# Kernel optimization log

Hardware: AMD Instinct MI355X
Metric: run time of the kernel (lower is better)

The kernel has to match this reference:

```python
import jax, jax.numpy as jnp
import numpy as np

DIM = 1280
HEADS = 16
HD = DIM // HEADS  # 80
NSEG = 8
LSEG = 1024
SEQ = NSEG * LSEG  # 8192


def _rotate_half(x):
    x1, x2 = jnp.split(x, 2, axis=-1)
    return jnp.concatenate([-x2, x1], axis=-1)


def setup_inputs() -> dict:
    key = jax.random.key(0)
    ks = jax.random.split(key, 6)
    hidden_states = jax.random.normal(ks[0], (SEQ, DIM), dtype=jnp.float32)
    # rotary embedding table: per-position angles over head_dim
    inv_freq = 1.0 / (10000.0 ** (np.arange(0, HD, 2, dtype=np.float32) / HD))
    pos = np.arange(SEQ, dtype=np.float32)
    freqs = np.outer(pos, inv_freq)                    # [SEQ, HD/2]
    emb = np.concatenate([freqs, freqs], axis=-1)      # [SEQ, HD]
    cos = jnp.asarray(np.cos(emb), dtype=jnp.float32)
    sin = jnp.asarray(np.sin(emb), dtype=jnp.float32)
    w_scale = 1.0 / np.sqrt(DIM)
    qkv_w = jax.random.normal(ks[1], (DIM, 3 * DIM), dtype=jnp.float32) * w_scale
    qkv_b = jax.random.normal(ks[2], (3 * DIM,), dtype=jnp.float32) * 0.02
    proj_w = jax.random.normal(ks[3], (DIM, DIM), dtype=jnp.float32) * w_scale
    proj_b = jax.random.normal(ks[4], (DIM,), dtype=jnp.float32) * 0.02
    cu_seqlens = jnp.arange(NSEG + 1, dtype=jnp.int32) * LSEG
    return {
        "hidden_states": hidden_states,
        "cos": cos,
        "sin": sin,
        "qkv_w": qkv_w,
        "qkv_b": qkv_b,
        "proj_w": proj_w,
        "proj_b": proj_b,
        "cu_seqlens": cu_seqlens,
    }


def reference(hidden_states, cos, sin, qkv_w, qkv_b, proj_w, proj_b, cu_seqlens):
    S, D = hidden_states.shape
    n_seg = cu_seqlens.shape[0] - 1          # static
    L = S // n_seg                            # equal-length packed segments
    # fused QKV projection: [S, 3D] -> q, k, v each [S, H, hd]
    qkv = hidden_states @ qkv_w + qkv_b
    q, k, v = (t.reshape(S, HEADS, HD) for t in jnp.split(qkv, 3, axis=-1))
    # RoPE (computed in fp32, as in apply_rotary_pos_emb_vision)
    c = cos.astype(jnp.float32)[:, None, :]   # [S, 1, hd]
    s = sin.astype(jnp.float32)[:, None, :]
    qf = q.astype(jnp.float32)
    kf = k.astype(jnp.float32)
    q = (qf * c + _rotate_half(qf) * s).astype(q.dtype)
    k = (kf * c + _rotate_half(kf) * s).astype(k.dtype)
    # block-diagonal varlen attention == independent attention per segment
    qs = q.reshape(n_seg, L, HEADS, HD)
    ks = k.reshape(n_seg, L, HEADS, HD)
    vs = v.reshape(n_seg, L, HEADS, HD)
    scale = HD ** -0.5
    scores = jnp.einsum("nqhd,nkhd->nhqk", qs, ks) * scale
    probs = jax.nn.softmax(scores.astype(jnp.float32), axis=-1).astype(qs.dtype)
    out = jnp.einsum("nhqk,nkhd->nqhd", probs, vs)     # [n, L, H, hd]
    out = out.reshape(S, D)
    return out @ proj_w + proj_b
```

## Files before the change

kernel.cpp:

```cpp
#include <hip/hip_runtime.h>

#define SEQ   8192
#define DIM   1280
#define HEADS 16
#define HD    80
#define LSEG  1024
#define QKVD  3840

typedef unsigned short USHORT;
typedef __attribute__((ext_vector_type(8))) short bf16x8;
typedef __attribute__((ext_vector_type(4))) float f32x4;
typedef __attribute__((ext_vector_type(4))) USHORT u16x4;
typedef __attribute__((ext_vector_type(2))) unsigned uint2v;

#define CSF  0.16129832f
#define DTHR 71.554175f

__device__ __forceinline__ USHORT f2bf(float x) {
  unsigned u = __float_as_uint(x);
  u += 0x7fffu + ((u >> 16) & 1u);
  return (USHORT)(u >> 16);
}
__device__ __forceinline__ float bf2f(USHORT b) {
  return __uint_as_float(((unsigned)b) << 16);
}
__device__ __forceinline__ void gload16(const void* g, void* l) {
  __builtin_amdgcn_global_load_lds(
      (const __attribute__((address_space(1))) void*)g,
      (__attribute__((address_space(3))) void*)l, 16, 0, 0);
}
__device__ __forceinline__ unsigned cvtpk(float a, float b) {
  unsigned d;
  asm("v_cvt_pk_bf16_f32 %0, %1, %2" : "=v"(d) : "v"(a), "v"(b));
  return d;
}

__global__ __launch_bounds__(256) void conv_f2b(const float* __restrict__ in,
                                                USHORT* __restrict__ out, int n4) {
  int i = blockIdx.x * 256 + threadIdx.x;
  if (i >= n4) return;
  float4 v = reinterpret_cast<const float4*>(in)[i];
  USHORT* o = out + (size_t)i * 4;
  o[0] = f2bf(v.x); o[1] = f2bf(v.y); o[2] = f2bf(v.z); o[3] = f2bf(v.w);
}

__global__ __launch_bounds__(256) void conv_transpose(const float* __restrict__ W,
                                                      USHORT* __restrict__ Th,
                                                      int K, int N) {
  __shared__ float t[32][33];
  const int n0 = blockIdx.x * 32, k0 = blockIdx.y * 32;
  const int c = threadIdx.x & 31, r0 = threadIdx.x >> 5;
  for (int r = r0; r < 32; r += 8) t[r][c] = W[(size_t)(k0 + r) * N + n0 + c];
  __syncthreads();
  for (int r = r0; r < 32; r += 8)
    Th[(size_t)(n0 + r) * K + k0 + c] = f2bf(t[c][r]);
}

__global__ __launch_bounds__(256) void vtrans(const USHORT* __restrict__ qkv,
                                              USHORT* __restrict__ VtG) {
  __shared__ USHORT t[32][33];
  const int c0 = blockIdx.x * 32, s0 = blockIdx.y * 32;
  const int c = threadIdx.x & 31, r0 = threadIdx.x >> 5;
  for (int r = r0; r < 32; r += 8)
    t[r][c] = qkv[(size_t)(s0 + r) * QKVD + 2 * DIM + c0 + c];
  __syncthreads();
  for (int r = r0; r < 32; r += 8)
    VtG[(size_t)(c0 + r) * SEQ + s0 + c] = t[c][r];
}

template <int OUTBF>
__global__ __launch_bounds__(256) void mfma_gemm(
    const USHORT* __restrict__ Ah, const USHORT* __restrict__ Bh,
    const float* __restrict__ bias, void* __restrict__ Cout,
    int M, int N, int K, int lda) {
  __shared__ __align__(16) USHORT AhL[2][8192];
  __shared__ __align__(16) USHORT BhL[2][8192];

  const int tid = threadIdx.x;
  const int l = tid & 63;
  const int w = tid >> 6;
  const int nrow = M >> 7;
  const int nwg = nrow * (N >> 7);
  const int orig = blockIdx.x;
  const int wg = (orig & 7) * (nwg >> 3) + (orig >> 3);
  const int row0 = (wg % nrow) << 7;
  const int col0 = (wg / nrow) << 7;
  const int wr = (w >> 1) << 6;
  const int wc = (w & 1) << 6;

  const f32x4 fz = {0.f, 0.f, 0.f, 0.f};
  f32x4 acc[4][4];
#pragma unroll
  for (int m = 0; m < 4; ++m)
#pragma unroll
    for (int n = 0; n < 4; ++n) acc[m][n] = fz;

  const int fr = l & 15;
  const int g = l >> 4;

  const int NT = K >> 6;

  auto stage = [&](int t, int b) {
    const int k0 = t << 6;
#pragma unroll
    for (int i = 0; i < 4; ++i) {
      const int u = (w * 4 + i) * 64 + l;
      const int row = u >> 3;
      const int c = (u & 7) ^ (row & 7);
      gload16(Ah + (size_t)(row0 + row) * lda + k0 + c * 8,
              &AhL[b][(w * 4 + i) * 512]);
      gload16(Bh + (size_t)(col0 + row) * K + k0 + c * 8,
              &BhL[b][(w * 4 + i) * 512]);
    }
  };

  stage(0, 0);
  stage(1, 1);

  for (int t = 0; t < NT; ++t) {
    const int cur = t & 1;
    asm volatile("s_waitcnt vmcnt(8)" ::: "memory");
    __builtin_amdgcn_sched_barrier(0);
    __builtin_amdgcn_s_barrier();
    __builtin_amdgcn_sched_barrier(0);
    bf16x8 ah[2][4], bh[2][4];
#pragma unroll
    for (int ks = 0; ks < 2; ++ks)
#pragma unroll
      for (int m = 0; m < 4; ++m) {
        const int sl = (((ks << 2) + g) ^ (fr & 7)) << 3;
        ah[ks][m] = *(const bf16x8*)&AhL[cur][(wr + m * 16 + fr) * 64 + sl];
        bh[ks][m] = *(const bf16x8*)&BhL[cur][(wc + m * 16 + fr) * 64 + sl];
      }
    asm volatile("s_waitcnt lgkmcnt(0)" ::: "memory");
    __builtin_amdgcn_sched_barrier(0);
    __builtin_amdgcn_s_barrier();
    __builtin_amdgcn_sched_barrier(0);
    const int tn = (t + 2 < NT) ? t + 2 : t;
    stage(tn, cur);
    __builtin_amdgcn_sched_barrier(0);
    __builtin_amdgcn_s_setprio(1);
#pragma unroll
    for (int ks = 0; ks < 2; ++ks)
#pragma unroll
      for (int m = 0; m < 4; ++m)
#pragma unroll
        for (int n = 0; n < 4; ++n)
          acc[m][n] = __builtin_amdgcn_mfma_f32_16x16x32_bf16(
              ah[ks][m], bh[ks][n], acc[m][n], 0, 0, 0);
    __builtin_amdgcn_s_setprio(0);
  }

  asm volatile("s_waitcnt vmcnt(0)" ::: "memory");

  float bv[4];
#pragma unroll
  for (int n = 0; n < 4; ++n) bv[n] = bias[col0 + wc + n * 16 + fr];
#pragma unroll
  for (int m = 0; m < 4; ++m)
#pragma unroll
    for (int n = 0; n < 4; ++n)
#pragma unroll
      for (int r = 0; r < 4; ++r) {
        const float v = acc[m][n][r] + bv[n];
        const int row = row0 + wr + m * 16 + (l >> 4) * 4 + r;
        const int col = col0 + wc + n * 16 + fr;
        if (OUTBF)
          ((USHORT*)Cout)[(size_t)row * N + col] = f2bf(v);
        else
          ((float*)Cout)[(size_t)row * N + col] = v;
      }
}

__global__ __launch_bounds__(256) void rope_b(USHORT* __restrict__ qkv,
                                              const float* __restrict__ cosb,
                                              const float* __restrict__ sinb) {
  int idx = blockIdx.x * 256 + threadIdx.x;
  const int d4 = (idx % 10) * 4;
  int t = idx / 10;
  const int h = t % HEADS;
  t /= HEADS;
  const int qk = t & 1;
  const int s = t >> 1;
  USHORT* base = qkv + (size_t)s * QKVD + qk * DIM + h * HD;
  const u16x4 x1 = *(const u16x4*)&base[d4];
  const u16x4 x2 = *(const u16x4*)&base[d4 + 40];
  const f32x4 c1 = *(const f32x4*)&cosb[s * HD + d4];
  const f32x4 s1 = *(const f32x4*)&sinb[s * HD + d4];
  const f32x4 c2 = *(const f32x4*)&cosb[s * HD + d4 + 40];
  const f32x4 s2 = *(const f32x4*)&sinb[s * HD + d4 + 40];
  u16x4 o1, o2;
#pragma unroll
  for (int j = 0; j < 4; ++j) {
    const float a = bf2f(x1[j]), b = bf2f(x2[j]);
    o1[j] = f2bf(a * c1[j] - b * s1[j]);
    o2[j] = f2bf(b * c2[j] + a * s2[j]);
  }
  *(u16x4*)&base[d4] = o1;
  *(u16x4*)&base[d4 + 40] = o2;
}

__global__ void zero_ws(uint4* z) {
  z[threadIdx.x] = uint4{0u, 0u, 0u, 0u};
}

__global__ __launch_bounds__(256) void attn_mfma6(const USHORT* __restrict__ qkv,
                                                  const USHORT* __restrict__ VtG,
                                                  const USHORT* __restrict__ zbuf,
                                                  USHORT* __restrict__ aoB) {
  const int h = blockIdx.y;
  const int bx = blockIdx.x;
  const int qb = (bx & 7) * 8 + (bx >> 3);
  const int s0 = qb * 128;
  const int k0g = (s0 / LSEG) * LSEG;
  const int tid = threadIdx.x;
  const int w = tid >> 6, l = tid & 63;
  const int g = l >> 4, fr = l & 15;
  const int q0 = s0 + w * 32;

  __shared__ __align__(16) USHORT Kl[2][64 * 128];
  __shared__ __align__(16) USHORT Vl[2][6144];
  __shared__ __align__(16) USHORT Pl[4][32 * 72];

  bf16x8 qb_frag[2][3];
#pragma unroll
  for (int nt2 = 0; nt2 < 2; ++nt2)
#pragma unroll
    for (int ks = 0; ks < 3; ++ks)
      qb_frag[nt2][ks] = *(const bf16x8*)
          &qkv[(size_t)(q0 + nt2 * 16 + fr) * QKVD + h * HD + ks * 32 + g * 8];

  const f32x4 fz = {0.f, 0.f, 0.f, 0.f};
  f32x4 oacc[2][5];
#pragma unroll
  for (int m = 0; m < 2; ++m)
#pragma unroll
    for (int n = 0; n < 5; ++n) oacc[m][n] = fz;
  float m_run[2] = {-3e38f, -3e38f};
  float l_run[2] = {0.f, 0.f};

  auto stageKV = [&](int kb, int b) {
    const size_t krow0 = (size_t)(k0g + kb * 64);
#pragma unroll
    for (int i = 0; i < 4; ++i) {
      const int t = (w * 4 + i) * 64 + l;
      const int row = t >> 4, c2 = t & 15, c = c2 ^ (row & 7);
      const USHORT* src =
          (c < 10) ? &qkv[(krow0 + row) * QKVD + DIM + h * HD + c * 8] : zbuf;
      gload16(src, &Kl[b][(w * 4 + i) * 512]);
    }
#pragma unroll
    for (int i = 0; i < 3; ++i) {
      const int u = (w * 3 + i) * 64 + l;
      const int s = u / 9, r8 = u - s * 9;
      const USHORT* src = (r8 < 8 && s < 80)
          ? &VtG[(size_t)(h * HD + s) * SEQ + krow0 + r8 * 8] : zbuf;
      gload16(src, &Vl[b][(w * 3 + i) * 512]);
    }
  };

  stageKV(0, 0);
  stageKV(1, 1);

  for (int kb = 0; kb < 16; ++kb) {
    const int cur = kb & 1;
    asm volatile("s_waitcnt vmcnt(7)" ::: "memory");
    __builtin_amdgcn_sched_barrier(0);
    __builtin_amdgcn_s_barrier();
    __builtin_amdgcn_sched_barrier(0);

    f32x4 sc[4][2];
#pragma unroll
    for (int m = 0; m < 4; ++m)
#pragma unroll
      for (int nt2 = 0; nt2 < 2; ++nt2) sc[m][nt2] = fz;
#pragma unroll
    for (int ks = 0; ks < 3; ++ks)
#pragma unroll
      for (int m = 0; m < 4; ++m) {
        const bf16x8 kbf = *(const bf16x8*)
            &Kl[cur][(m * 16 + fr) * 128 + ((4 * ks + g) ^ (fr & 7)) * 8];
#pragma unroll
        for (int nt2 = 0; nt2 < 2; ++nt2)
          sc[m][nt2] = __builtin_amdgcn_mfma_f32_16x16x32_bf16(
              kbf, qb_frag[nt2][ks], sc[m][nt2], 0, 0, 0);
      }

    float rmax[2];
#pragma unroll
    for (int nt2 = 0; nt2 < 2; ++nt2) {
      float mx = -3e38f;
#pragma unroll
      for (int m = 0; m < 4; ++m)
#pragma unroll
        for (int j = 0; j < 4; ++j) mx = fmaxf(mx, sc[m][nt2][j]);
      mx = fmaxf(mx, __shfl_xor(mx, 16));
      mx = fmaxf(mx, __shfl_xor(mx, 32));
      rmax[nt2] = mx;
    }
    const bool need =
        (rmax[0] > m_run[0] + DTHR) || (rmax[1] > m_run[1] + DTHR);
    if (__any(need)) {
      float fac[2];
#pragma unroll
      for (int nt2 = 0; nt2 < 2; ++nt2) {
        const float mn = fmaxf(m_run[nt2], rmax[nt2]);
        fac[nt2] = exp2f((m_run[nt2] - mn) * CSF);
        m_run[nt2] = mn;
        l_run[nt2] *= fac[nt2];
      }
#pragma unroll
      for (int mt2 = 0; mt2 < 2; ++mt2)
#pragma unroll
        for (int j = 0; j < 4; ++j) {
          const float fb = __shfl(fac[mt2], 20 * g + j);
#pragma unroll
          for (int nt = 0; nt < 5; ++nt) oacc[mt2][nt][j] *= fb;
        }
    }
#pragma unroll
    for (int nt2 = 0; nt2 < 2; ++nt2) {
      const float mcs = m_run[nt2] * CSF;
      float ps = 0.f;
#pragma unroll
      for (int m = 0; m < 4; ++m) {
        float p[4];
#pragma unroll
        for (int j = 0; j < 4; ++j) {
          p[j] = exp2f(sc[m][nt2][j] * CSF - mcs);
          ps += p[j];
        }
        const uint2v pw = {cvtpk(p[0], p[1]), cvtpk(p[2], p[3])};
        *(uint2v*)&Pl[w][(nt2 * 16 + fr) * 72 + m * 16 + g * 4] = pw;
      }
      ps += __shfl_xor(ps, 16);
      ps += __shfl_xor(ps, 32);
      l_run[nt2] += ps;
    }

#pragma unroll
    for (int ks = 0; ks < 2; ++ks) {
      bf16x8 pa[2];
#pragma unroll
      for (int mt2 = 0; mt2 < 2; ++mt2)
        pa[mt2] = *(const bf16x8*)&Pl[w][(mt2 * 16 + fr) * 72 + ks * 32 + g * 8];
#pragma unroll
      for (int nt = 0; nt < 5; ++nt) {
        const bf16x8 vb =
            *(const bf16x8*)&Vl[cur][(nt * 16 + fr) * 72 + ks * 32 + g * 8];
#pragma unroll
        for (int mt2 = 0; mt2 < 2; ++mt2)
          oacc[mt2][nt] = __builtin_amdgcn_mfma_f32_16x16x32_bf16(
              pa[mt2], vb, oacc[mt2][nt], 0, 0, 0);
      }
    }

    __builtin_amdgcn_s_barrier();
    __builtin_amdgcn_sched_barrier(0);
    const int kn = (kb + 2 < 16) ? kb + 2 : kb;
    stageKV(kn, cur);
    __builtin_amdgcn_sched_barrier(0);
  }

  asm volatile("s_waitcnt vmcnt(0)" ::: "memory");

  float linv[2][4];
#pragma unroll
  for (int mt2 = 0; mt2 < 2; ++mt2)
#pragma unroll
    for (int j = 0; j < 4; ++j)
      linv[mt2][j] = 1.f / __shfl(l_run[mt2], 20 * g + j);
#pragma unroll
  for (int mt2 = 0; mt2 < 2; ++mt2)
#pragma unroll
    for (int nt = 0; nt < 5; ++nt)
#pragma unroll
      for (int j = 0; j < 4; ++j) {
        const int row = s0 + w * 32 + mt2 * 16 + g * 4 + j;
        const int col = h * HD + nt * 16 + fr;
        aoB[(size_t)row * QKVD + col] = f2bf(oacc[mt2][nt][j] * linv[mt2][j]);
      }
}

extern "C" void kernel_launch(void* const* d_in, const int* in_sizes, int n_in,
                              void* d_out, int out_size, void* d_ws,
                              size_t ws_size, hipStream_t stream) {
  const float* hs = (const float*)d_in[0];
  const float* cosb = (const float*)d_in[1];
  const float* sinb = (const float*)d_in[2];
  const float* qkv_w = (const float*)d_in[3];
  const float* qkv_b = (const float*)d_in[4];
  const float* proj_w = (const float*)d_in[5];
  const float* proj_b = (const float*)d_in[6];
  char* ws = (char*)d_ws;

  USHORT* qkvB  = (USHORT*)(ws);
  USHORT* hsB   = (USHORT*)(ws + 62914560u);
  USHORT* qkvwT = (USHORT*)(ws + 83886080u);
  USHORT* pwT   = (USHORT*)(ws + 93716480u);
  USHORT* VtG   = hsB;
  USHORT* zbuf  = qkvwT;
  USHORT* aoB   = qkvB + 2 * DIM;

  conv_f2b<<<SEQ * DIM / 4 / 256, 256, 0, stream>>>(hs, hsB, SEQ * DIM / 4);
  conv_transpose<<<dim3(QKVD / 32, DIM / 32), 256, 0, stream>>>(
      qkv_w, qkvwT, DIM, QKVD);
  conv_transpose<<<dim3(DIM / 32, DIM / 32), 256, 0, stream>>>(
      proj_w, pwT, DIM, DIM);

  mfma_gemm<1><<<(SEQ / 128) * (QKVD / 128), 256, 0, stream>>>(
      hsB, qkvwT, qkv_b, qkvB, SEQ, QKVD, DIM, DIM);
  rope_b<<<SEQ * HEADS * 2 * 10 / 256, 256, 0, stream>>>(qkvB, cosb, sinb);
  vtrans<<<dim3(DIM / 32, SEQ / 32), 256, 0, stream>>>(qkvB, VtG);
  zero_ws<<<1, 64, 0, stream>>>((uint4*)zbuf);
  attn_mfma6<<<dim3(SEQ / 128, HEADS), 256, 0, stream>>>(qkvB, VtG, zbuf, aoB);
  mfma_gemm<0><<<(SEQ / 128) * (DIM / 128), 256, 0, stream>>>(
      aoB, pwT, proj_b, d_out, SEQ, DIM, DIM, QKVD);
}
```

Before: 311.6 us.

## Use 256x256-tile 512-thread MFMA GEMM for QKV projection

Adds a new GEMM kernel with 256x256 output tiles, 8 waves per block, 128KB dynamic LDS, double-buffered K=64 staging with XOR swizzle, and uses it for the QKV projection. Larger tiles raise arithmetic intensity and cut global reloads of A and B. The cost is fewer workgroups (480) and higher register and LDS pressure, which may limit occupancy. The launch_bounds(512,2) requests two blocks per CU, which 128KB of LDS per block would not allow.

```diff
diff --git a/kernel.cpp b/kernel.cpp
--- a/kernel.cpp
+++ b/kernel.cpp
@@ -66,6 +66,109 @@
   __syncthreads();
   for (int r = r0; r < 32; r += 8)
     VtG[(size_t)(c0 + r) * SEQ + s0 + c] = t[c][r];
+}
+
+__global__ __launch_bounds__(512, 2) void mfma_gemm256(
+    const USHORT* __restrict__ Ah, const USHORT* __restrict__ Bh,
+    const float* __restrict__ bias, USHORT* __restrict__ Cout,
+    int M, int N, int K, int lda) {
+  extern __shared__ USHORT sm[];
+
+  const int tid = threadIdx.x;
+  const int l = tid & 63;
+  const int w = tid >> 6;
+  const int fr = l & 15;
+  const int g = l >> 4;
+  const int nrow = M >> 8;
+  const int nwg = nrow * (N >> 8);
+  const int orig = blockIdx.x;
+  const int wg = (orig & 7) * (nwg >> 3) + (orig >> 3);
+  const int row0 = (wg % nrow) << 8;
+  const int col0 = (wg / nrow) << 8;
+  const int wr = (w >> 2) << 7;
+  const int wc = (w & 3) << 6;
+
+  const f32x4 fz = {0.f, 0.f, 0.f, 0.f};
+  f32x4 acc[8][4];
+#pragma unroll
+  for (int m = 0; m < 8; ++m)
+#pragma unroll
+    for (int n = 0; n < 4; ++n) acc[m][n] = fz;
+
+  const int NT = K >> 6;
+
+  auto stage = [&](int t, int b) {
+    const int k0 = t << 6;
+#pragma unroll
+    for (int i = 0; i < 4; ++i) {
+      const int u = i * 512 + tid;
+      const int row = u >> 3;
+      const int c = (u & 7) ^ (row & 7);
+      USHORT* dst = sm + (i * 512 + (w << 6)) * 8;
+      gload16(Ah + (size_t)(row0 + row) * lda + k0 + c * 8,
+              dst + b * 16384);
+      gload16(Bh + (size_t)(col0 + row) * K + k0 + c * 8,
+              dst + 32768 + b * 16384);
+    }
+  };
+
+  stage(0, 0);
+  stage(1, 1);
+
+  for (int t = 0; t < NT; ++t) {
+    const int cur = t & 1;
+    asm volatile("s_waitcnt vmcnt(8)" ::: "memory");
+    __builtin_amdgcn_sched_barrier(0);
+    __builtin_amdgcn_s_barrier();
+    __builtin_amdgcn_sched_barrier(0);
+    bf16x8 ah[2][8], bh[2][4];
+#pragma unroll
+    for (int ks = 0; ks < 2; ++ks) {
+      const int sl = (((ks << 2) + g) ^ (fr & 7)) << 3;
+#pragma unroll
+      for (int m = 0; m < 8; ++m)
+        ah[ks][m] = *(const bf16x8*)
+            &sm[cur * 16384 + (wr + m * 16 + fr) * 64 + sl];
+#pragma unroll
+      for (int n = 0; n < 4; ++n)
+        bh[ks][n] = *(const bf16x8*)
+            &sm[32768 + cur * 16384 + (wc + n * 16 + fr) * 64 + sl];
+    }
+    asm volatile("s_waitcnt lgkmcnt(0)" ::: "memory");
+    __builtin_amdgcn_sched_barrier(0);
+    __builtin_amdgcn_s_barrier();
+    __builtin_amdgcn_sched_barrier(0);
+    const int tn = (t + 2 < NT) ? t + 2 : t;
+    stage(tn, cur);
+    __builtin_amdgcn_sched_barrier(0);
+    __builtin_amdgcn_s_setprio(1);
+#pragma unroll
+    for (int ks = 0; ks < 2; ++ks)
+#pragma unroll
+      for (int m = 0; m < 8; ++m)
+#pragma unroll
+        for (int n = 0; n < 4; ++n)
+          acc[m][n] = __builtin_amdgcn_mfma_f32_16x16x32_bf16(
+              ah[ks][m], bh[ks][n], acc[m][n], 0, 0, 0);
+    __builtin_amdgcn_s_setprio(0);
+  }
+
+  asm volatile("s_waitcnt vmcnt(0)" ::: "memory");
+
+  float bv[4];
+#pragma unroll
+  for (int n = 0; n < 4; ++n) bv[n] = bias[col0 + wc + n * 16 + fr];
+#pragma unroll
+  for (int m = 0; m < 8; ++m)
+#pragma unroll
+    for (int n = 0; n < 4; ++n)
+#pragma unroll
+      for (int r = 0; r < 4; ++r) {
+        const float v = acc[m][n][r] + bv[n];
+        const int row = row0 + wr + m * 16 + g * 4 + r;
+        const int col = col0 + wc + n * 16 + fr;
+        Cout[(size_t)row * N + col] = f2bf(v);
+      }
 }
 
 template <int OUTBF>
@@ -402,13 +505,16 @@
   USHORT* zbuf  = qkvwT;
   USHORT* aoB   = qkvB + 2 * DIM;
 
+  hipFuncSetAttribute((const void*)mfma_gemm256,
+                      hipFuncAttributeMaxDynamicSharedMemorySize, 131072);
+
   conv_f2b<<<SEQ * DIM / 4 / 256, 256, 0, stream>>>(hs, hsB, SEQ * DIM / 4);
   conv_transpose<<<dim3(QKVD / 32, DIM / 32), 256, 0, stream>>>(
       qkv_w, qkvwT, DIM, QKVD);
   conv_transpose<<<dim3(DIM / 32, DIM / 32), 256, 0, stream>>>(
       proj_w, pwT, DIM, DIM);
 
-  mfma_gemm<1><<<(SEQ / 128) * (QKVD / 128), 256, 0, stream>>>(
+  mfma_gemm256<<<(SEQ / 256) * (QKVD / 256), 512, 131072, stream>>>(
       hsB, qkvwT, qkv_b, qkvB, SEQ, QKVD, DIM, DIM);
   rope_b<<<SEQ * HEADS * 2 * 10 / 256, 256, 0, stream>>>(qkvB, cosb, sinb);
   vtrans<<<dim3(DIM / 32, SEQ / 32), 256, 0, stream>>>(qkvB, VtG);
```

Measured after the change: 290.0 us. 6.9% less time.
